# Kernel optimization log

Hardware: AMD Instinct MI355X
Metric: run time of the kernel (lower is better)

Reference implementation:

```python
import jax, jax.numpy as jnp
import numpy as np
import math

D_MODEL = 512
N_HEADS = 8
WINDOW = 5
B, S = 4, 2048


def setup_inputs() -> dict:
    key = jax.random.key(0)
    ks = jax.random.split(key, 16)
    d = D_MODEL

    def lin(k, fan_in, fan_out):
        bound = 1.0 / math.sqrt(fan_in)
        kw, kb = jax.random.split(k)
        W = jax.random.uniform(kw, (fan_in, fan_out), jnp.float32, -bound, bound)
        b = jax.random.uniform(kb, (fan_out,), jnp.float32, -bound, bound)
        return W, b

    x = jax.random.normal(ks[0], (B, S, d), jnp.float32)
    W1, b1 = lin(ks[1], d, 2 * d)      # mapping layer 1
    W2, b2 = lin(ks[2], 2 * d, d)      # mapping layer 2
    Wq, bq = lin(ks[3], d, d)
    Wk, bk = lin(ks[4], d, d)
    Wv, bv = lin(ks[5], d, d)
    Wo, bo = lin(ks[6], d, d)
    return dict(x=x, W1=W1, b1=b1, W2=W2, b2=b2, Wq=Wq, bq=bq,
                Wk=Wk, bk=bk, Wv=Wv, bv=bv, Wo=Wo, bo=bo)


def reference(x, W1, b1, W2, b2, Wq, bq, Wk, bk, Wv, bv, Wo, bo):
    Bsz, S_, d = x.shape
    h = N_HEADS
    hd = d // h

    # mapping MLP: Linear -> ReLU -> Linear
    xm = jax.nn.relu(x @ W1 + b1) @ W2 + b2

    def split_heads(t):  # [B,S,d] -> [B,h,S,hd]
        return t.reshape(Bsz, S_, h, hd).transpose(0, 2, 1, 3)

    Q = split_heads(xm @ Wq + bq)
    K = split_heads(xm @ Wk + bk)
    V = split_heads(xm @ Wv + bv)

    scores = jnp.einsum('bhqd,bhkd->bhqk', Q, K) / math.sqrt(hd)

    # inverse sliding-window mask: positions with |i-j| <= window are EXCLUDED
    idx = jnp.arange(S_)
    adjacent = jnp.abs(idx[:, None] - idx[None, :]) <= WINDOW  # [S,S] bool
    scores = jnp.where(adjacent[None, None], -1e9, scores)

    attn = jax.nn.softmax(scores, axis=-1)
    out = jnp.einsum('bhqk,bhkd->bhqd', attn, V)
    out = out.transpose(0, 2, 1, 3).reshape(Bsz, S_, d)
    return out @ Wo + bo
```

## Files before the change

kernel.cpp:

```cpp
#include <hip/hip_runtime.h>
#include <stdint.h>

typedef __attribute__((ext_vector_type(8))) short bf16x8;
typedef __attribute__((ext_vector_type(4))) float f32x4;

__device__ __forceinline__ float bf2f(uint16_t u) {
    union { uint32_t u; float f; } c; c.u = ((uint32_t)u) << 16; return c.f;
}
__device__ __forceinline__ uint16_t f2bf(float f) {
    union { float f; uint32_t u; } c; c.f = f;
    uint32_t r = c.u + 0x7fffu + ((c.u >> 16) & 1u);
    return (uint16_t)(r >> 16);
}
__device__ __forceinline__ uint32_t pk2bf(float a, float b) {
#if __has_builtin(__builtin_amdgcn_cvt_pk_bf16_f32)
    auto v = __builtin_amdgcn_cvt_pk_bf16_f32(a, b);
    uint32_t u; __builtin_memcpy(&u, &v, 4); return u;
#else
    return (uint32_t)f2bf(a) | ((uint32_t)f2bf(b) << 16);
#endif
}
__device__ __forceinline__ float fexp2(float x) {
#if __has_builtin(__builtin_amdgcn_exp2f)
    return __builtin_amdgcn_exp2f(x);
#else
    return exp2f(x);
#endif
}

__device__ __forceinline__ void gld_lds16(const uint16_t* g, uint16_t* l) {
    __builtin_amdgcn_global_load_lds(
        (const __attribute__((address_space(1))) void*)g,
        (__attribute__((address_space(3))) void*)l, 16, 0, 0);
}

__global__ void prep_all(const float* __restrict__ x,
                         const float* __restrict__ W1, const float* __restrict__ W2,
                         const float* __restrict__ Wq, const float* __restrict__ Wk,
                         const float* __restrict__ Wv, const float* __restrict__ Wo,
                         const float* __restrict__ b1, const float* __restrict__ b2,
                         const float* __restrict__ bq, const float* __restrict__ bk,
                         const float* __restrict__ bv, const float* __restrict__ bo,
                         uint16_t* __restrict__ W1T, uint16_t* __restrict__ W2T,
                         uint16_t* __restrict__ WqkvT, uint16_t* __restrict__ WoT,
                         uint16_t* __restrict__ xb, uint16_t* __restrict__ bbase)
{
    const int id = blockIdx.x;
    const int tx = threadIdx.x, ty = threadIdx.y;
    const int tid = ty * 32 + tx;
    if (id < 2048) {
        __shared__ uint16_t t[32][33];
        const float* src; uint16_t* dst; int R, C, tile;
        if      (id < 512)  { src = W1; dst = W1T;              R = 512;  C = 1024; tile = id; }
        else if (id < 1024) { src = W2; dst = W2T;              R = 1024; C = 512;  tile = id - 512; }
        else if (id < 1280) { src = Wq; dst = WqkvT;            R = 512;  C = 512;  tile = id - 1024; }
        else if (id < 1536) { src = Wk; dst = WqkvT + 512*512;  R = 512;  C = 512;  tile = id - 1280; }
        else if (id < 1792) { src = Wv; dst = WqkvT + 1024*512; R = 512;  C = 512;  tile = id - 1536; }
        else                { src = Wo; dst = WoT;              R = 512;  C = 512;  tile = id - 1792; }
        const int ntx = C / 32;
        const int bx = (tile % ntx) * 32, by = (tile / ntx) * 32;
#pragma unroll
        for (int i = ty; i < 32; i += 8) t[i][tx] = f2bf(src[(size_t)(by + i) * C + bx + tx]);
        __syncthreads();
#pragma unroll
        for (int i = ty; i < 32; i += 8) dst[(size_t)(bx + i) * R + by + tx] = t[tx][i];
    } else if (id < 6144) {
        int i = (id - 2048) * 256 + tid;
        float4 v = ((const float4*)x)[i];
        ushort4 o;
        o.x = f2bf(v.x); o.y = f2bf(v.y); o.z = f2bf(v.z); o.w = f2bf(v.w);
        ((ushort4*)xb)[i] = o;
    } else {
        int i = (id - 6144) * 256 + tid;
        if      (i < 1024) bbase[i] = f2bf(b1[i]);
        else if (i < 1536) bbase[i] = f2bf(b2[i - 1024]);
        else if (i < 2048) bbase[i] = f2bf(bq[i - 1536]);
        else if (i < 2560) bbase[i] = f2bf(bk[i - 2048]);
        else if (i < 3072) bbase[i] = f2bf(bv[i - 2560]);
        else if (i < 3584) bbase[i] = f2bf(bo[i - 3072]);
    }
}

template<int RELU, int F32OUT>
__global__ __launch_bounds__(256)
void gemm_k(const uint16_t* __restrict__ A, const uint16_t* __restrict__ Bt,
            const uint16_t* __restrict__ bias, void* __restrict__ Cv,
            int M, int N, int K)
{
    __shared__ __align__(16) uint16_t lsA[128 * 64];
    __shared__ __align__(16) uint16_t lsB[128 * 64];

    const int tid = threadIdx.x, lane = tid & 63;
    const int wid = tid >> 6;
    const int quad = lane >> 4, lm = lane & 15;
    const int wm = wid >> 1, wn = wid & 1;
    const int m0 = blockIdx.y * 128, n0 = blockIdx.x * 128;

    f32x4 acc[4][4];
#pragma unroll
    for (int i = 0; i < 4; ++i)
#pragma unroll
        for (int j = 0; j < 4; ++j) acc[i][j] = (f32x4){0.f, 0.f, 0.f, 0.f};

    for (int k0 = 0; k0 < K; k0 += 64) {
        __syncthreads();
#pragma unroll
        for (int c4 = 0; c4 < 4; ++c4) {
            const int chunk = c4 * 256 + tid;
            const int r = chunk >> 3, lc = (chunk & 7) ^ (r & 7);
            gld_lds16(A  + (size_t)(m0 + r) * K + k0 + lc * 8, lsA + (size_t)chunk * 8);
            gld_lds16(Bt + (size_t)(n0 + r) * K + k0 + lc * 8, lsB + (size_t)chunk * 8);
        }
        __syncthreads();

#pragma unroll
        for (int kh = 0; kh < 2; ++kh) {
            bf16x8 af[4], bfr[4];
#pragma unroll
            for (int t = 0; t < 4; ++t) {
                const int pcA = ((kh * 4 + quad) ^ (lm & 7));
                af[t]  = *(const bf16x8*)(lsA + (wm * 64 + t * 16 + lm) * 64 + pcA * 8);
                bfr[t] = *(const bf16x8*)(lsB + (wn * 64 + t * 16 + lm) * 64 + pcA * 8);
            }
#pragma unroll
            for (int i = 0; i < 4; ++i)
#pragma unroll
                for (int j = 0; j < 4; ++j)
                    acc[i][j] = __builtin_amdgcn_mfma_f32_16x16x32_bf16(af[i], bfr[j], acc[i][j], 0, 0, 0);
        }
    }

#pragma unroll
    for (int i = 0; i < 4; ++i) {
        const int r0 = m0 + wm * 64 + i * 16 + quad * 4;
#pragma unroll
        for (int j = 0; j < 4; ++j) {
            const int col = n0 + wn * 64 + j * 16 + lm;
            const float bvj = bf2f(bias[col]);
#pragma unroll
            for (int r = 0; r < 4; ++r) {
                float v = acc[i][j][r] + bvj;
                if (RELU) v = fmaxf(v, 0.f);
                if (F32OUT) ((float*)Cv)[(size_t)(r0 + r) * N + col] = v;
                else        ((uint16_t*)Cv)[(size_t)(r0 + r) * N + col] = f2bf(v);
            }
        }
    }
}

template<int RELU, int F32OUT>
__global__ __launch_bounds__(256)
void gemm_k64(const uint16_t* __restrict__ A, const uint16_t* __restrict__ Bt,
              const uint16_t* __restrict__ bias, void* __restrict__ Cv,
              int M, int N, int K)
{
    __shared__ __align__(16) uint16_t lsA[64 * 64];
    __shared__ __align__(16) uint16_t lsB[128 * 64];

    const int tid = threadIdx.x, lane = tid & 63;
    const int wid = tid >> 6;
    const int quad = lane >> 4, lm = lane & 15;
    const int wm = wid >> 1, wn = wid & 1;
    const int m0 = blockIdx.y * 64, n0 = blockIdx.x * 128;

    f32x4 acc[2][4];
#pragma unroll
    for (int i = 0; i < 2; ++i)
#pragma unroll
        for (int j = 0; j < 4; ++j) acc[i][j] = (f32x4){0.f, 0.f, 0.f, 0.f};

    for (int k0 = 0; k0 < K; k0 += 64) {
        __syncthreads();
#pragma unroll
        for (int c4 = 0; c4 < 2; ++c4) {
            const int chunk = c4 * 256 + tid;
            const int r = chunk >> 3, lc = (chunk & 7) ^ (r & 7);
            gld_lds16(A + (size_t)(m0 + r) * K + k0 + lc * 8, lsA + (size_t)chunk * 8);
        }
#pragma unroll
        for (int c4 = 0; c4 < 4; ++c4) {
            const int chunk = c4 * 256 + tid;
            const int r = chunk >> 3, lc = (chunk & 7) ^ (r & 7);
            gld_lds16(Bt + (size_t)(n0 + r) * K + k0 + lc * 8, lsB + (size_t)chunk * 8);
        }
        __syncthreads();

#pragma unroll
        for (int kh = 0; kh < 2; ++kh) {
            const int pc = ((kh * 4 + quad) ^ (lm & 7));
            bf16x8 af[2], bfr[4];
#pragma unroll
            for (int t = 0; t < 2; ++t)
                af[t] = *(const bf16x8*)(lsA + (wm * 32 + t * 16 + lm) * 64 + pc * 8);
#pragma unroll
            for (int t = 0; t < 4; ++t)
                bfr[t] = *(const bf16x8*)(lsB + (wn * 64 + t * 16 + lm) * 64 + pc * 8);
#pragma unroll
            for (int i = 0; i < 2; ++i)
#pragma unroll
                for (int j = 0; j < 4; ++j)
                    acc[i][j] = __builtin_amdgcn_mfma_f32_16x16x32_bf16(af[i], bfr[j], acc[i][j], 0, 0, 0);
        }
    }

#pragma unroll
    for (int i = 0; i < 2; ++i) {
        const int r0 = m0 + wm * 32 + i * 16 + quad * 4;
#pragma unroll
        for (int j = 0; j < 4; ++j) {
            const int col = n0 + wn * 64 + j * 16 + lm;
            const float bvj = bf2f(bias[col]);
#pragma unroll
            for (int r = 0; r < 4; ++r) {
                float v = acc[i][j][r] + bvj;
                if (RELU) v = fmaxf(v, 0.f);
                if (F32OUT) ((float*)Cv)[(size_t)(r0 + r) * N + col] = v;
                else        ((uint16_t*)Cv)[(size_t)(r0 + r) * N + col] = f2bf(v);
            }
        }
    }
}

__global__ __launch_bounds__(256)
void gemm_qkv_s(const uint16_t* __restrict__ A, const uint16_t* __restrict__ Bt,
                const uint16_t* __restrict__ bq, const uint16_t* __restrict__ bk,
                const uint16_t* __restrict__ bv_,
                uint16_t* __restrict__ qk, uint16_t* __restrict__ Vt)
{
    __shared__ __align__(16) uint16_t lsA[128 * 64];
    __shared__ __align__(16) uint16_t lsB[128 * 64];

    const int tid = threadIdx.x, lane = tid & 63;
    const int wid = tid >> 6;
    const int quad = lane >> 4, lm = lane & 15;
    const int wm = wid >> 1, wn = wid & 1;
    const int m0 = blockIdx.y * 128, n0 = blockIdx.x * 128;
    const int part = n0 >> 9;
    const uint16_t* B = (part == 0) ? bq : (part == 1) ? bk : bv_;
    const int K = 512;

    f32x4 acc[4][4];
#pragma unroll
    for (int i = 0; i < 4; ++i)
#pragma unroll
        for (int j = 0; j < 4; ++j) acc[i][j] = (f32x4){0.f, 0.f, 0.f, 0.f};

    for (int k0 = 0; k0 < K; k0 += 64) {
        __syncthreads();
#pragma unroll
        for (int c4 = 0; c4 < 4; ++c4) {
            const int chunk = c4 * 256 + tid;
            const int r = chunk >> 3, lc = (chunk & 7) ^ (r & 7);
            gld_lds16(A  + (size_t)(m0 + r) * K + k0 + lc * 8, lsA + (size_t)chunk * 8);
            gld_lds16(Bt + (size_t)(n0 + r) * K + k0 + lc * 8, lsB + (size_t)chunk * 8);
        }
        __syncthreads();

#pragma unroll
        for (int kh = 0; kh < 2; ++kh) {
            const int pc = ((kh * 4 + quad) ^ (lm & 7));
            bf16x8 af[4], bfr[4];
#pragma unroll
            for (int t = 0; t < 4; ++t) {
                af[t]  = *(const bf16x8*)(lsA + (wm * 64 + t * 16 + lm) * 64 + pc * 8);
                bfr[t] = *(const bf16x8*)(lsB + (wn * 64 + t * 16 + lm) * 64 + pc * 8);
            }
#pragma unroll
            for (int i = 0; i < 4; ++i)
#pragma unroll
                for (int j = 0; j < 4; ++j)
                    acc[i][j] = __builtin_amdgcn_mfma_f32_16x16x32_bf16(af[i], bfr[j], acc[i][j], 0, 0, 0);
        }
    }

#pragma unroll
    for (int i = 0; i < 4; ++i) {
        const int mb = m0 + wm * 64 + i * 16 + quad * 4;
#pragma unroll
        for (int j = 0; j < 4; ++j) {
            const int nl = (n0 & 511) + wn * 64 + j * 16 + lm;
            const float bvj = bf2f(B[nl]);
            if (part < 2) {
#pragma unroll
                for (int r = 0; r < 4; ++r)
                    qk[(size_t)(mb + r) * 1024 + part * 512 + nl] = f2bf(acc[i][j][r] + bvj);
            } else {
                const int h = nl >> 6, d = nl & 63;
                const int b = mb >> 11, s0 = mb & 2047;
                const size_t base = ((size_t)(((b << 3) | h)) * 64 + d) * 2048 + s0;
#pragma unroll
                for (int r = 0; r < 4; ++r)
                    Vt[base + r] = f2bf(acc[i][j][r] + bvj);
            }
        }
    }
}

__global__ __launch_bounds__(256, 2)
void attn_k(const uint16_t* __restrict__ qk, const uint16_t* __restrict__ Vt,
            uint16_t* __restrict__ Out)
{
    __shared__ __align__(16) uint16_t lsK[128 * 64];
    __shared__ __align__(16) uint16_t lsV[64 * 128];
    __shared__ __align__(16) uint16_t lsP[128 * 136];

    const int tid = threadIdx.x, lane = tid & 63, wid = tid >> 6;
    const int quad = lane >> 4, lm = lane & 15;
    const int bh = blockIdx.y, b = bh >> 3, h = bh & 7;
    const int q0 = blockIdx.x * 128;
    const float cscale = 0.125f * 1.44269504088896f;

    bf16x8 qf[2][2];
#pragma unroll
    for (int i = 0; i < 2; ++i)
#pragma unroll
        for (int ks = 0; ks < 2; ++ks) {
            bf16x8 q = *(const bf16x8*)(qk +
                (size_t)(b * 2048 + q0 + wid * 32 + i * 16 + lm) * 1024 + h * 64 + ks * 32 + quad * 8);
#pragma unroll
            for (int e = 0; e < 8; ++e)
                q[e] = (short)f2bf(bf2f((uint16_t)q[e]) * cscale);
            qf[i][ks] = q;
        }

    f32x4 oacc[2][4];
#pragma unroll
    for (int i = 0; i < 2; ++i)
#pragma unroll
        for (int n = 0; n < 4; ++n) oacc[i][n] = (f32x4){0.f, 0.f, 0.f, 0.f};
    float lrow[2][4];
#pragma unroll
    for (int i = 0; i < 2; ++i)
#pragma unroll
        for (int r = 0; r < 4; ++r) lrow[i][r] = 0.f;

    for (int j0 = 0; j0 < 2048; j0 += 128) {
        __syncthreads();
#pragma unroll
        for (int c4 = 0; c4 < 4; ++c4) {
            const int chunk = c4 * 256 + tid;
            const int r = chunk >> 3, lc = (chunk & 7) ^ (r & 7);
            gld_lds16(qk + (size_t)(b * 2048 + j0 + r) * 1024 + 512 + h * 64 + lc * 8,
                      lsK + (size_t)chunk * 8);
        }
#pragma unroll
        for (int c4 = 0; c4 < 4; ++c4) {
            const int chunk = c4 * 256 + tid;
            const int d = chunk >> 4, lc = (chunk & 15) ^ (d & 15);
            gld_lds16(Vt + (size_t)(bh * 64 + d) * 2048 + j0 + lc * 8,
                      lsV + (size_t)chunk * 8);
        }
        __syncthreads();

        f32x4 sacc[2][8];
#pragma unroll
        for (int i = 0; i < 2; ++i)
#pragma unroll
            for (int j = 0; j < 8; ++j) sacc[i][j] = (f32x4){0.f, 0.f, 0.f, 0.f};
#pragma unroll
        for (int ks = 0; ks < 2; ++ks)
#pragma unroll
            for (int j = 0; j < 8; ++j) {
                const int pc = (ks * 4 + quad) ^ (lm & 7);
                bf16x8 kf = *(const bf16x8*)(lsK + (j * 16 + lm) * 64 + pc * 8);
#pragma unroll
                for (int i = 0; i < 2; ++i)
                    sacc[i][j] = __builtin_amdgcn_mfma_f32_16x16x32_bf16(qf[i][ks], kf, sacc[i][j], 0, 0, 0);
            }

        if ((j0 + 127 >= q0 - 5) && (j0 <= q0 + 127 + 5)) {
#pragma unroll
            for (int i = 0; i < 2; ++i)
#pragma unroll
                for (int j = 0; j < 8; ++j)
#pragma unroll
                    for (int r = 0; r < 4; ++r) {
                        int qr = q0 + wid * 32 + i * 16 + quad * 4 + r;
                        int kc = j0 + j * 16 + lm;
                        int dd = qr - kc; if (dd < 0) dd = -dd;
                        if (dd <= 5) sacc[i][j][r] = -1e30f;
                    }
        }

#pragma unroll
        for (int i = 0; i < 2; ++i)
#pragma unroll
            for (int r = 0; r < 4; ++r) {
                const int prow = wid * 32 + i * 16 + quad * 4 + r;
                float p[8], rs = 0.f;
#pragma unroll
                for (int j = 0; j < 8; ++j) { p[j] = fexp2(sacc[i][j][r]); rs += p[j]; }
                lrow[i][r] += rs;
#pragma unroll
                for (int jp = 0; jp < 4; ++jp) {
                    uint32_t u = pk2bf(p[2 * jp], p[2 * jp + 1]);
                    lsP[prow * 136 + (2 * jp) * 16 + lm]     = (uint16_t)u;
                    lsP[prow * 136 + (2 * jp + 1) * 16 + lm] = (uint16_t)(u >> 16);
                }
            }

#pragma unroll
        for (int ks = 0; ks < 4; ++ks) {
            bf16x8 pa[2];
#pragma unroll
            for (int i = 0; i < 2; ++i)
                pa[i] = *(const bf16x8*)(lsP + (wid * 32 + i * 16 + lm) * 136 + ks * 32 + quad * 8);
#pragma unroll
            for (int n = 0; n < 4; ++n) {
                const int pc = (ks * 4 + quad) ^ lm;
                bf16x8 vf = *(const bf16x8*)(lsV + (n * 16 + lm) * 128 + pc * 8);
#pragma unroll
                for (int i = 0; i < 2; ++i)
                    oacc[i][n] = __builtin_amdgcn_mfma_f32_16x16x32_bf16(pa[i], vf, oacc[i][n], 0, 0, 0);
            }
        }
    }

#pragma unroll
    for (int i = 0; i < 2; ++i)
#pragma unroll
        for (int r = 0; r < 4; ++r) {
            float l = lrow[i][r];
            l += __shfl_xor(l, 1, 16);
            l += __shfl_xor(l, 2, 16);
            l += __shfl_xor(l, 4, 16);
            l += __shfl_xor(l, 8, 16);
            const float inv = 1.f / (l + 1e-30f);
            const int s = q0 + wid * 32 + i * 16 + quad * 4 + r;
#pragma unroll
            for (int n = 0; n < 4; ++n)
                Out[(size_t)(b * 2048 + s) * 512 + h * 64 + n * 16 + lm] = f2bf(oacc[i][n][r] * inv);
        }
}

extern "C" void kernel_launch(void* const* d_in, const int* in_sizes, int n_in,
                              void* d_out, int out_size, void* d_ws, size_t ws_size,
                              hipStream_t stream)
{
    const float* x  = (const float*)d_in[0];
    const float* W1 = (const float*)d_in[1];
    const float* b1 = (const float*)d_in[2];
    const float* W2 = (const float*)d_in[3];
    const float* b2 = (const float*)d_in[4];
    const float* Wq = (const float*)d_in[5];
    const float* bq = (const float*)d_in[6];
    const float* Wk = (const float*)d_in[7];
    const float* bk = (const float*)d_in[8];
    const float* Wv = (const float*)d_in[9];
    const float* bv = (const float*)d_in[10];
    const float* Wo = (const float*)d_in[11];
    const float* bo = (const float*)d_in[12];
    (void)in_sizes; (void)n_in; (void)out_size; (void)ws_size;

    char* ws = (char*)d_ws;
    const size_t MiB = 1024 * 1024;
    uint16_t* xb    = (uint16_t*)(ws + 0);
    uint16_t* W1T   = (uint16_t*)(ws + 8 * MiB);
    uint16_t* W2T   = (uint16_t*)(ws + 9 * MiB);
    uint16_t* WqkvT = (uint16_t*)(ws + 10 * MiB);
    uint16_t* WoT   = (uint16_t*)(ws + 11 * MiB + 512 * 1024);
    uint16_t* bbase = (uint16_t*)(ws + 12 * MiB);
    uint16_t* b1b = bbase, *b2b = bbase + 1024, *bqb = bbase + 1536;
    uint16_t* bkb = bbase + 2048, *bvb = bbase + 2560, *bob = bbase + 3072;
    uint16_t* xm1   = (uint16_t*)(ws + 13 * MiB);
    uint16_t* xm    = (uint16_t*)(ws + 29 * MiB);
    uint16_t* qk    = xm1;
    uint16_t* att   = xm;
    uint16_t* Vt    = xb;

    prep_all<<<6158, dim3(32, 8), 0, stream>>>(x, W1, W2, Wq, Wk, Wv, Wo,
                                               b1, b2, bq, bk, bv, bo,
                                               W1T, W2T, WqkvT, WoT, xb, bbase);

    gemm_k<1,0>  <<<dim3(8, 64),  256, 0, stream>>>(xb,  W1T, b1b, xm1, 8192, 1024, 512);
    gemm_k64<0,0><<<dim3(4, 128), 256, 0, stream>>>(xm1, W2T, b2b, xm,  8192, 512, 1024);
    gemm_qkv_s   <<<dim3(12, 64), 256, 0, stream>>>(xm, WqkvT, bqb, bkb, bvb, qk, Vt);
    attn_k       <<<dim3(16, 32), 256, 0, stream>>>(qk, Vt, att);
    gemm_k64<0,1><<<dim3(4, 128), 256, 0, stream>>>(att, WoT, bob, d_out, 8192, 512, 512);
}
```

Before: 225.0 us.

## Keep softmax probabilities in registers via transposed QK MFMA and permuted V layout

Swaps the MFMA operands in the QK^T product so each lane holds a transposed score tile. The exponentiated scores can then be packed directly into the A-operand fragment for the PV MFMA, instead of round-tripping through a shared-memory P buffer. To match the register layout, the V-transpose writer permutes sequence positions within each 32-element group, and the row-sum reduction changes to cross-quad shuffles plus a broadcast. Dropping the large LDS P buffer lets the launch bound request 4 blocks per SM for higher occupancy, at the cost of tighter register limits.

```diff
diff --git a/kernel.cpp b/kernel.cpp
--- a/kernel.cpp
+++ b/kernel.cpp
@@ -287,7 +287,8 @@
             } else {
                 const int h = nl >> 6, d = nl & 63;
                 const int b = mb >> 11, s0 = mb & 2047;
-                const size_t base = ((size_t)(((b << 3) | h)) * 64 + d) * 2048 + s0;
+                const int sp = (s0 & ~31) | ((s0 & 12) << 1) | (((s0 >> 4) & 1) << 2);
+                const size_t base = ((size_t)(((b << 3) | h)) * 64 + d) * 2048 + sp;
 #pragma unroll
                 for (int r = 0; r < 4; ++r)
                     Vt[base + r] = f2bf(acc[i][j][r] + bvj);
@@ -296,13 +297,12 @@
     }
 }
 
-__global__ __launch_bounds__(256, 2)
+__global__ __launch_bounds__(256, 4)
 void attn_k(const uint16_t* __restrict__ qk, const uint16_t* __restrict__ Vt,
             uint16_t* __restrict__ Out)
 {
     __shared__ __align__(16) uint16_t lsK[128 * 64];
     __shared__ __align__(16) uint16_t lsV[64 * 128];
-    __shared__ __align__(16) uint16_t lsP[128 * 136];
 
     const int tid = threadIdx.x, lane = tid & 63, wid = tid >> 6;
     const int quad = lane >> 4, lm = lane & 15;
@@ -328,11 +328,7 @@
     for (int i = 0; i < 2; ++i)
 #pragma unroll
         for (int n = 0; n < 4; ++n) oacc[i][n] = (f32x4){0.f, 0.f, 0.f, 0.f};
-    float lrow[2][4];
-#pragma unroll
-    for (int i = 0; i < 2; ++i)
-#pragma unroll
-        for (int r = 0; r < 4; ++r) lrow[i][r] = 0.f;
+    float lrow[2] = {0.f, 0.f};
 
     for (int j0 = 0; j0 < 2048; j0 += 128) {
         __syncthreads();
@@ -365,46 +361,45 @@
                 bf16x8 kf = *(const bf16x8*)(lsK + (j * 16 + lm) * 64 + pc * 8);
 #pragma unroll
                 for (int i = 0; i < 2; ++i)
-                    sacc[i][j] = __builtin_amdgcn_mfma_f32_16x16x32_bf16(qf[i][ks], kf, sacc[i][j], 0, 0, 0);
+                    sacc[i][j] = __builtin_amdgcn_mfma_f32_16x16x32_bf16(kf, qf[i][ks], sacc[i][j], 0, 0, 0);
             }
 
         if ((j0 + 127 >= q0 - 5) && (j0 <= q0 + 127 + 5)) {
 #pragma unroll
-            for (int i = 0; i < 2; ++i)
+            for (int i = 0; i < 2; ++i) {
+                const int qr = q0 + wid * 32 + i * 16 + lm;
 #pragma unroll
                 for (int j = 0; j < 8; ++j)
 #pragma unroll
                     for (int r = 0; r < 4; ++r) {
-                        int qr = q0 + wid * 32 + i * 16 + quad * 4 + r;
-                        int kc = j0 + j * 16 + lm;
+                        int kc = j0 + j * 16 + quad * 4 + r;
                         int dd = qr - kc; if (dd < 0) dd = -dd;
                         if (dd <= 5) sacc[i][j][r] = -1e30f;
                     }
-        }
-
-#pragma unroll
-        for (int i = 0; i < 2; ++i)
-#pragma unroll
-            for (int r = 0; r < 4; ++r) {
-                const int prow = wid * 32 + i * 16 + quad * 4 + r;
-                float p[8], rs = 0.f;
-#pragma unroll
-                for (int j = 0; j < 8; ++j) { p[j] = fexp2(sacc[i][j][r]); rs += p[j]; }
-                lrow[i][r] += rs;
-#pragma unroll
-                for (int jp = 0; jp < 4; ++jp) {
-                    uint32_t u = pk2bf(p[2 * jp], p[2 * jp + 1]);
-                    lsP[prow * 136 + (2 * jp) * 16 + lm]     = (uint16_t)u;
-                    lsP[prow * 136 + (2 * jp + 1) * 16 + lm] = (uint16_t)(u >> 16);
-                }
-            }
+            }
+        }
 
 #pragma unroll
         for (int ks = 0; ks < 4; ++ks) {
             bf16x8 pa[2];
 #pragma unroll
-            for (int i = 0; i < 2; ++i)
-                pa[i] = *(const bf16x8*)(lsP + (wid * 32 + i * 16 + lm) * 136 + ks * 32 + quad * 8);
+            for (int i = 0; i < 2; ++i) {
+                const float p0 = fexp2(sacc[i][2 * ks + 0][0]);
+                const float p1 = fexp2(sacc[i][2 * ks + 0][1]);
+                const float p2 = fexp2(sacc[i][2 * ks + 0][2]);
+                const float p3 = fexp2(sacc[i][2 * ks + 0][3]);
+                const float p4 = fexp2(sacc[i][2 * ks + 1][0]);
+                const float p5 = fexp2(sacc[i][2 * ks + 1][1]);
+                const float p6 = fexp2(sacc[i][2 * ks + 1][2]);
+                const float p7 = fexp2(sacc[i][2 * ks + 1][3]);
+                lrow[i] += ((p0 + p1) + (p2 + p3)) + ((p4 + p5) + (p6 + p7));
+                union { bf16x8 v; uint32_t u[4]; } c;
+                c.u[0] = pk2bf(p0, p1);
+                c.u[1] = pk2bf(p2, p3);
+                c.u[2] = pk2bf(p4, p5);
+                c.u[3] = pk2bf(p6, p7);
+                pa[i] = c.v;
+            }
 #pragma unroll
             for (int n = 0; n < 4; ++n) {
                 const int pc = (ks * 4 + quad) ^ lm;
@@ -417,20 +412,20 @@
     }
 
 #pragma unroll
-    for (int i = 0; i < 2; ++i)
+    for (int i = 0; i < 2; ++i) {
+        float l = lrow[i];
+        l += __shfl_xor(l, 16);
+        l += __shfl_xor(l, 32);
+        const float inv = 1.f / (l + 1e-30f);
 #pragma unroll
         for (int r = 0; r < 4; ++r) {
-            float l = lrow[i][r];
-            l += __shfl_xor(l, 1, 16);
-            l += __shfl_xor(l, 2, 16);
-            l += __shfl_xor(l, 4, 16);
-            l += __shfl_xor(l, 8, 16);
-            const float inv = 1.f / (l + 1e-30f);
+            const float invr = __shfl(inv, quad * 4 + r, 16);
             const int s = q0 + wid * 32 + i * 16 + quad * 4 + r;
 #pragma unroll
             for (int n = 0; n < 4; ++n)
-                Out[(size_t)(b * 2048 + s) * 512 + h * 64 + n * 16 + lm] = f2bf(oacc[i][n][r] * inv);
-        }
+                Out[(size_t)(b * 2048 + s) * 512 + h * 64 + n * 16 + lm] = f2bf(oacc[i][n][r] * invr);
+        }
+    }
 }
 
 extern "C" void kernel_launch(void* const* d_in, const int* in_sizes, int n_in,
```

Result: slower. 298.5 us (+32.7%).
